# Performance work log

Hardware: AMD Instinct MI355X
Metric: run time of the kernel (lower is better)

Reference implementation:

```python
import jax, jax.numpy as jnp
import numpy as np

N = 100000  # number of nodes
E = 3200000  # number of edges (avg degree 32)


def spmm(rows, cols, vals, Y):
    # sparse A (COO) @ dense Y : gather rows of Y at cols, scale, scatter-add to rows
    return jax.ops.segment_sum(vals[:, None] * Y[cols], rows, num_segments=N)


def setup_inputs() -> dict:
    key = jax.random.key(0)
    kx, kr, kc, kv, k0, k1 = jax.random.split(key, 6)
    X = jax.random.normal(kx, (N, 512), dtype=jnp.float32)
    edge_rows = jax.random.randint(kr, (E,), 0, N, dtype=jnp.int32)
    edge_cols = jax.random.randint(kc, (E,), 0, N, dtype=jnp.int32)
    edge_vals = jax.random.uniform(kv, (E,), dtype=jnp.float32)
    W0 = jax.random.normal(k0, (512, 256), dtype=jnp.float32) * 0.05
    W1 = jax.random.normal(k1, (256, 64), dtype=jnp.float32) * 0.05
    return {"X": X, "edge_rows": edge_rows, "edge_cols": edge_cols,
            "edge_vals": edge_vals, "W0": W0, "W1": W1}


def reference(X, edge_rows, edge_cols, edge_vals, W0, W1):
    # layer 1: A_hat @ (X W0), relu
    H1 = jax.nn.relu(spmm(edge_rows, edge_cols, edge_vals, X @ W0))  # [N, H]
    # layer 2: A_hat @ (H1 W1), softmax over classes
    Z = spmm(edge_rows, edge_cols, edge_vals, H1 @ W1)  # [N, F]
    return jax.nn.softmax(Z, axis=-1)
```

## Files before the change

kernel.cpp:

```cpp
#include <hip/hip_runtime.h>
#include <hip/hip_bf16.h>
#include <hip/hip_fp16.h>
#include <cstdint>

#define N_NODES 100000
#define N_EDGES 3200000
#define F_IN    512
#define F_HID   256
#define F_OUT   64
#define CAP     96

#define NSHARD   4
#define SHARD_SZ 25000
#define G_SCATTER 12500
#define NSLICE   4
#define LDS_STRIDE 272

typedef _Float16 half8_t __attribute__((ext_vector_type(8)));
typedef _Float16 half4_t __attribute__((ext_vector_type(4)));
typedef float    float4_t __attribute__((ext_vector_type(4)));


__global__ __launch_bounds__(256) void prep_kernel(
    const float* __restrict__ W0, const float* __restrict__ W1,
    _Float16* __restrict__ W0T, _Float16* __restrict__ W1T,
    int* __restrict__ cursor) {
    int i = blockIdx.x * 256 + threadIdx.x;
    if (i < N_NODES) cursor[i] = 0;
    if (i < F_HID * F_IN) {
        int n = i >> 9, k = i & 511;
        W0T[i] = (_Float16)W0[k * F_HID + n];
    }
    int j = i - F_HID * F_IN;
    if (j >= 0 && j < F_OUT * F_HID) {
        int n = j >> 8, k = j & 255;
        W1T[j] = (_Float16)W1[k * F_OUT + n];
    }
}


__global__ __launch_bounds__(256) void ell_scatter_kernel(
    const int* __restrict__ erows, const int* __restrict__ ecols,
    const float* __restrict__ evals, int* __restrict__ cursor,
    int2* __restrict__ ell) {
    const int shard = blockIdx.x / G_SCATTER;
    const int e = (blockIdx.x % G_SCATTER) * 256 + threadIdx.x;
    int r = erows[e];
    if (r / SHARD_SZ != shard) return;
    int p = atomicAdd(&cursor[r], 1);
    if (p < CAP)
        ell[(size_t)r * CAP + p] = make_int2(ecols[e], __float_as_int(evals[e]));
}


__global__ __launch_bounds__(256) void gemm1_mfma_kernel(
    const float* __restrict__ X, const _Float16* __restrict__ W0T,
    _Float16* __restrict__ H0) {
    const int wave = threadIdx.x >> 6;
    const int lane = threadIdx.x & 63;
    const int l15  = lane & 15;
    const int quad = lane >> 4;
    const int m0   = blockIdx.x * 64;
    const int n0   = wave * 64;

    float4_t acc[4][4] = {};

    int row[4];
    #pragma unroll
    for (int mt = 0; mt < 4; mt++) {
        int r = m0 + mt * 16 + l15;
        row[mt] = r < N_NODES ? r : N_NODES - 1;
    }

    for (int k0 = 0; k0 < F_IN; k0 += 32) {
        const int kk = k0 + quad * 8;
        half8_t b[4];
        #pragma unroll
        for (int nt = 0; nt < 4; nt++)
            b[nt] = *(const half8_t*)(W0T + (size_t)(n0 + nt * 16 + l15) * F_IN + kk);

        half8_t a[4];
        #pragma unroll
        for (int mt = 0; mt < 4; mt++) {
            const float* p = X + (size_t)row[mt] * F_IN + kk;
            float4_t lo = *(const float4_t*)p;
            float4_t hi = *(const float4_t*)(p + 4);
            half8_t f;
            f[0] = (_Float16)lo[0]; f[1] = (_Float16)lo[1];
            f[2] = (_Float16)lo[2]; f[3] = (_Float16)lo[3];
            f[4] = (_Float16)hi[0]; f[5] = (_Float16)hi[1];
            f[6] = (_Float16)hi[2]; f[7] = (_Float16)hi[3];
            a[mt] = f;
        }

        #pragma unroll
        for (int mt = 0; mt < 4; mt++)
            #pragma unroll
            for (int nt = 0; nt < 4; nt++)
                acc[mt][nt] = __builtin_amdgcn_mfma_f32_16x16x32_f16(
                    a[mt], b[nt], acc[mt][nt], 0, 0, 0);
    }

    #pragma unroll
    for (int mt = 0; mt < 4; mt++)
        #pragma unroll
        for (int reg = 0; reg < 4; reg++) {
            int m = m0 + mt * 16 + quad * 4 + reg;
            if (m < N_NODES) {
                #pragma unroll
                for (int nt = 0; nt < 4; nt++)
                    H0[((size_t)wave * N_NODES + m) * 64 + nt * 16 + l15] =
                        (_Float16)acc[mt][nt][reg];
            }
        }
}


__global__ __launch_bounds__(256) void spmm_relu_gemm2_kernel(
    const _Float16* __restrict__ H0, const int2* __restrict__ ell,
    const int* __restrict__ cursor, const _Float16* __restrict__ W1T,
    _Float16* __restrict__ H2) {
    __shared__ _Float16 hrow[16][LDS_STRIDE];

    const int t    = threadIdx.x & 63;
    const int grp  = threadIdx.x >> 4;
    const int sub  = threadIdx.x & 15;
    const int base = blockIdx.x * 16;
    const int r    = base + grp;

    int n = cursor[r]; if (n > CAP) n = CAP;
    const int2* cv = ell + (size_t)r * CAP;

    for (int s = 0; s < NSLICE; s++) {
        const half4_t* slab = (const half4_t*)(H0 + (size_t)s * N_NODES * 64);
        float4_t acc = {};
        int j = 0;
        for (; j + 4 <= n; j += 4) {
            int4 e0 = *(const int4*)(cv + j);
            int4 e1 = *(const int4*)(cv + j + 2);
            half4_t g0 = slab[(size_t)e0.x * 16 + sub];
            half4_t g1 = slab[(size_t)e0.z * 16 + sub];
            half4_t g2 = slab[(size_t)e1.x * 16 + sub];
            half4_t g3 = slab[(size_t)e1.z * 16 + sub];
            float v0 = __int_as_float(e0.y), v1 = __int_as_float(e0.w);
            float v2 = __int_as_float(e1.y), v3 = __int_as_float(e1.w);
            #pragma unroll
            for (int i = 0; i < 4; i++) {
                acc[i] = fmaf(v0, (float)g0[i], acc[i]);
                acc[i] = fmaf(v1, (float)g1[i], acc[i]);
                acc[i] = fmaf(v2, (float)g2[i], acc[i]);
                acc[i] = fmaf(v3, (float)g3[i], acc[i]);
            }
        }
        for (; j < n; j++) {
            int2 e = cv[j];
            half4_t g = slab[(size_t)e.x * 16 + sub];
            float vv = __int_as_float(e.y);
            #pragma unroll
            for (int i = 0; i < 4; i++) acc[i] = fmaf(vv, (float)g[i], acc[i]);
        }
        half4_t o;
        #pragma unroll
        for (int i = 0; i < 4; i++) o[i] = (_Float16)fmaxf(acc[i], 0.f);
        *(half4_t*)(&hrow[grp][s * 64 + sub * 4]) = o;
    }
    __syncthreads();

    const int wave = threadIdx.x >> 6;
    const int l15  = t & 15;
    const int quad = t >> 4;
    float4_t acc2 = {};
    #pragma unroll
    for (int k0 = 0; k0 < F_HID; k0 += 32) {
        const int kk = k0 + quad * 8;
        half8_t a = *(const half8_t*)(&hrow[l15][kk]);
        half8_t b = *(const half8_t*)(W1T + (size_t)(wave * 16 + l15) * F_HID + kk);
        acc2 = __builtin_amdgcn_mfma_f32_16x16x32_f16(a, b, acc2, 0, 0, 0);
    }
    #pragma unroll
    for (int reg = 0; reg < 4; reg++) {
        int m = base + quad * 4 + reg;
        H2[(size_t)m * F_OUT + wave * 16 + l15] = (_Float16)acc2[reg];
    }
}


__global__ __launch_bounds__(256) void spmm_softmax_kernel(
    const _Float16* __restrict__ H2, const int2* __restrict__ ell,
    const int* __restrict__ cursor, float* __restrict__ out) {
    const int lane = threadIdx.x & 63;
    const int r = blockIdx.x * 4 + (threadIdx.x >> 6);
    int n = cursor[r]; if (n > CAP) n = CAP;
    const int2* cv = ell + (size_t)r * CAP;

    float acc = 0.f;
    int j = 0;
    for (; j + 4 <= n; j += 4) {
        int4 e0 = *(const int4*)(cv + j);
        int4 e1 = *(const int4*)(cv + j + 2);
        acc = fmaf(__int_as_float(e0.y), (float)H2[(size_t)e0.x * F_OUT + lane], acc);
        acc = fmaf(__int_as_float(e0.w), (float)H2[(size_t)e0.z * F_OUT + lane], acc);
        acc = fmaf(__int_as_float(e1.y), (float)H2[(size_t)e1.x * F_OUT + lane], acc);
        acc = fmaf(__int_as_float(e1.w), (float)H2[(size_t)e1.z * F_OUT + lane], acc);
    }
    for (; j < n; j++) {
        int2 e = cv[j];
        acc = fmaf(__int_as_float(e.y), (float)H2[(size_t)e.x * F_OUT + lane], acc);
    }

    float m = acc;
    #pragma unroll
    for (int o = 32; o >= 1; o >>= 1) m = fmaxf(m, __shfl_xor(m, o, 64));
    float e = expf(acc - m);
    float s = e;
    #pragma unroll
    for (int o = 32; o >= 1; o >>= 1) s += __shfl_xor(s, o, 64);
    out[(size_t)r * F_OUT + lane] = e / s;
}


extern "C" void kernel_launch(void* const* d_in, const int* in_sizes, int n_in,
                              void* d_out, int out_size, void* d_ws, size_t ws_size,
                              hipStream_t stream) {
    const float* X     = (const float*)d_in[0];
    const int*   erows = (const int*)  d_in[1];
    const int*   ecols = (const int*)  d_in[2];
    const float* evals = (const float*)d_in[3];
    const float* W0    = (const float*)d_in[4];
    const float* W1    = (const float*)d_in[5];
    float* out = (float*)d_out;

    char* p = (char*)d_ws;
    _Float16* H0  = (_Float16*)p; p += (size_t)N_NODES * F_HID * 2;
    _Float16* H2  = (_Float16*)p; p += (size_t)N_NODES * F_OUT * 2;
    _Float16* W0T = (_Float16*)p; p += (size_t)F_HID * F_IN * 2;
    _Float16* W1T = (_Float16*)p; p += (size_t)F_OUT * F_HID * 2;
    int*  cursor  = (int*)p;      p += (size_t)N_NODES * 4;
    int2* ell     = (int2*)p;

    prep_kernel<<<576, 256, 0, stream>>>(W0, W1, W0T, W1T, cursor);

    ell_scatter_kernel<<<NSHARD * G_SCATTER, 256, 0, stream>>>(
        erows, ecols, evals, cursor, ell);

    gemm1_mfma_kernel<<<(N_NODES + 63) / 64, 256, 0, stream>>>(X, W0T, H0);

    spmm_relu_gemm2_kernel<<<N_NODES / 16, 256, 0, stream>>>(H0, ell, cursor, W1T, H2);

    spmm_softmax_kernel<<<N_NODES / 4, 256, 0, stream>>>(H2, ell, cursor, out);
}
```

Measured before the change: 934.6 us.

## Pack ELL entries into 32-bit words and gather full hidden rows per wave

Each ELL entry now fits in one 32-bit word: the column index sits in the upper 17 bits and the edge value is stored as a 15-bit fp16 without its sign bit, replacing the 8-byte int2. H0 goes from four feature slices to a plain row-major [N,256] layout, so the first SpMM reads each neighbour's row once as a contiguous 512-byte gather per wave instead of four passes over separate slices. The scatter now uses 8 row shards interleaved by block index, and CAP grows to 128. The goal is less index traffic, fewer passes over the edge list and better gather coalescing. The cost is that edge values are rounded to fp16 and rely on being non-negative, and column indices must fit in 17 bits.

```diff
diff --git a/kernel.cpp b/kernel.cpp
--- a/kernel.cpp
+++ b/kernel.cpp
@@ -8,17 +8,20 @@
 #define F_IN    512
 #define F_HID   256
 #define F_OUT   64
-#define CAP     96
-
-#define NSHARD   4
-#define SHARD_SZ 25000
+#define CAP     128
+
+#define NSHARD   8
+#define SHARD_SZ 12500
 #define G_SCATTER 12500
-#define NSLICE   4
 #define LDS_STRIDE 272
 
 typedef _Float16 half8_t __attribute__((ext_vector_type(8)));
 typedef _Float16 half4_t __attribute__((ext_vector_type(4)));
 typedef float    float4_t __attribute__((ext_vector_type(4)));
+
+__device__ __forceinline__ float unpack_val(unsigned p) {
+    return (float)__builtin_bit_cast(_Float16, (unsigned short)(p & 0x7FFFu));
+}
 
 
 __global__ __launch_bounds__(256) void prep_kernel(
@@ -42,14 +45,16 @@
 __global__ __launch_bounds__(256) void ell_scatter_kernel(
     const int* __restrict__ erows, const int* __restrict__ ecols,
     const float* __restrict__ evals, int* __restrict__ cursor,
-    int2* __restrict__ ell) {
-    const int shard = blockIdx.x / G_SCATTER;
-    const int e = (blockIdx.x % G_SCATTER) * 256 + threadIdx.x;
+    unsigned* __restrict__ ell) {
+    const int shard = blockIdx.x & 7;
+    const int e = (blockIdx.x >> 3) * 256 + threadIdx.x;
     int r = erows[e];
     if (r / SHARD_SZ != shard) return;
     int p = atomicAdd(&cursor[r], 1);
-    if (p < CAP)
-        ell[(size_t)r * CAP + p] = make_int2(ecols[e], __float_as_int(evals[e]));
+    if (p < CAP) {
+        unsigned short hb = __builtin_bit_cast(unsigned short, (_Float16)evals[e]);
+        ell[(size_t)r * CAP + p] = ((unsigned)ecols[e] << 15) | (unsigned)hb;
+    }
 }
 
 
@@ -109,7 +114,7 @@
             if (m < N_NODES) {
                 #pragma unroll
                 for (int nt = 0; nt < 4; nt++)
-                    H0[((size_t)wave * N_NODES + m) * 64 + nt * 16 + l15] =
+                    H0[(size_t)m * F_HID + n0 + nt * 16 + l15] =
                         (_Float16)acc[mt][nt][reg];
             }
         }
@@ -117,33 +122,32 @@
 
 
 __global__ __launch_bounds__(256) void spmm_relu_gemm2_kernel(
-    const _Float16* __restrict__ H0, const int2* __restrict__ ell,
+    const _Float16* __restrict__ H0, const unsigned* __restrict__ ell,
     const int* __restrict__ cursor, const _Float16* __restrict__ W1T,
     _Float16* __restrict__ H2) {
     __shared__ _Float16 hrow[16][LDS_STRIDE];
 
+    const int wave = threadIdx.x >> 6;
     const int t    = threadIdx.x & 63;
-    const int grp  = threadIdx.x >> 4;
-    const int sub  = threadIdx.x & 15;
     const int base = blockIdx.x * 16;
-    const int r    = base + grp;
-
-    int n = cursor[r]; if (n > CAP) n = CAP;
-    const int2* cv = ell + (size_t)r * CAP;
-
-    for (int s = 0; s < NSLICE; s++) {
-        const half4_t* slab = (const half4_t*)(H0 + (size_t)s * N_NODES * 64);
+    const half4_t* H0v = (const half4_t*)H0;
+
+    for (int rr = 0; rr < 4; rr++) {
+        const int local = wave * 4 + rr;
+        const int r = base + local;
+        int n = cursor[r]; if (n > CAP) n = CAP;
+        const unsigned* cv = ell + (size_t)r * CAP;
+
         float4_t acc = {};
         int j = 0;
         for (; j + 4 <= n; j += 4) {
-            int4 e0 = *(const int4*)(cv + j);
-            int4 e1 = *(const int4*)(cv + j + 2);
-            half4_t g0 = slab[(size_t)e0.x * 16 + sub];
-            half4_t g1 = slab[(size_t)e0.z * 16 + sub];
-            half4_t g2 = slab[(size_t)e1.x * 16 + sub];
-            half4_t g3 = slab[(size_t)e1.z * 16 + sub];
-            float v0 = __int_as_float(e0.y), v1 = __int_as_float(e0.w);
-            float v2 = __int_as_float(e1.y), v3 = __int_as_float(e1.w);
+            uint4 e = *(const uint4*)(cv + j);
+            half4_t g0 = H0v[(size_t)(e.x >> 15) * 64 + t];
+            half4_t g1 = H0v[(size_t)(e.y >> 15) * 64 + t];
+            half4_t g2 = H0v[(size_t)(e.z >> 15) * 64 + t];
+            half4_t g3 = H0v[(size_t)(e.w >> 15) * 64 + t];
+            float v0 = unpack_val(e.x), v1 = unpack_val(e.y);
+            float v2 = unpack_val(e.z), v3 = unpack_val(e.w);
             #pragma unroll
             for (int i = 0; i < 4; i++) {
                 acc[i] = fmaf(v0, (float)g0[i], acc[i]);
@@ -153,20 +157,19 @@
             }
         }
         for (; j < n; j++) {
-            int2 e = cv[j];
-            half4_t g = slab[(size_t)e.x * 16 + sub];
-            float vv = __int_as_float(e.y);
+            unsigned e = cv[j];
+            half4_t g = H0v[(size_t)(e >> 15) * 64 + t];
+            float vv = unpack_val(e);
             #pragma unroll
             for (int i = 0; i < 4; i++) acc[i] = fmaf(vv, (float)g[i], acc[i]);
         }
         half4_t o;
         #pragma unroll
         for (int i = 0; i < 4; i++) o[i] = (_Float16)fmaxf(acc[i], 0.f);
-        *(half4_t*)(&hrow[grp][s * 64 + sub * 4]) = o;
+        *(half4_t*)(&hrow[local][t * 4]) = o;
     }
     __syncthreads();
 
-    const int wave = threadIdx.x >> 6;
     const int l15  = t & 15;
     const int quad = t >> 4;
     float4_t acc2 = {};
@@ -186,26 +189,25 @@
 
 
 __global__ __launch_bounds__(256) void spmm_softmax_kernel(
-    const _Float16* __restrict__ H2, const int2* __restrict__ ell,
+    const _Float16* __restrict__ H2, const unsigned* __restrict__ ell,
     const int* __restrict__ cursor, float* __restrict__ out) {
     const int lane = threadIdx.x & 63;
     const int r = blockIdx.x * 4 + (threadIdx.x >> 6);
     int n = cursor[r]; if (n > CAP) n = CAP;
-    const int2* cv = ell + (size_t)r * CAP;
+    const unsigned* cv = ell + (size_t)r * CAP;
 
     float acc = 0.f;
     int j = 0;
     for (; j + 4 <= n; j += 4) {
-        int4 e0 = *(const int4*)(cv + j);
-        int4 e1 = *(const int4*)(cv + j + 2);
-        acc = fmaf(__int_as_float(e0.y), (float)H2[(size_t)e0.x * F_OUT + lane], acc);
-        acc = fmaf(__int_as_float(e0.w), (float)H2[(size_t)e0.z * F_OUT + lane], acc);
-        acc = fmaf(__int_as_float(e1.y), (float)H2[(size_t)e1.x * F_OUT + lane], acc);
-        acc = fmaf(__int_as_float(e1.w), (float)H2[(size_t)e1.z * F_OUT + lane], acc);
+        uint4 e = *(const uint4*)(cv + j);
+        acc = fmaf(unpack_val(e.x), (float)H2[(size_t)(e.x >> 15) * F_OUT + lane], acc);
+        acc = fmaf(unpack_val(e.y), (float)H2[(size_t)(e.y >> 15) * F_OUT + lane], acc);
+        acc = fmaf(unpack_val(e.z), (float)H2[(size_t)(e.z >> 15) * F_OUT + lane], acc);
+        acc = fmaf(unpack_val(e.w), (float)H2[(size_t)(e.w >> 15) * F_OUT + lane], acc);
     }
     for (; j < n; j++) {
-        int2 e = cv[j];
-        acc = fmaf(__int_as_float(e.y), (float)H2[(size_t)e.x * F_OUT + lane], acc);
+        unsigned e = cv[j];
+        acc = fmaf(unpack_val(e), (float)H2[(size_t)(e >> 15) * F_OUT + lane], acc);
     }
 
     float m = acc;
@@ -235,8 +237,8 @@
     _Float16* H2  = (_Float16*)p; p += (size_t)N_NODES * F_OUT * 2;
     _Float16* W0T = (_Float16*)p; p += (size_t)F_HID * F_IN * 2;
     _Float16* W1T = (_Float16*)p; p += (size_t)F_OUT * F_HID * 2;
-    int*  cursor  = (int*)p;      p += (size_t)N_NODES * 4;
-    int2* ell     = (int2*)p;
+    int*      cursor = (int*)p;   p += (size_t)N_NODES * 4;
+    unsigned* ell    = (unsigned*)p;
 
     prep_kernel<<<576, 256, 0, stream>>>(W0, W1, W0T, W1T, cursor);
 
```

Result: no change. 938.9 us (+0.5%).
